# Kernel tuning notes

Measured on AMD Instinct MI355X. Metric: run time of the kernel, lower is better.

The kernel has to match this reference:

```python
import jax, jax.numpy as jnp
import numpy as np

B, S = 128, 512          # batch, sequence length
VOCAB, E, H = 50000, 300, 64  # vocab, embed dim, hidden_size (num conv filters)
KMAX = H // 2 + 2 - 1    # largest kernel height = (H-1)//2 + 2 = 33


def setup_inputs() -> dict:
    key = jax.random.key(0)
    ks = jax.random.split(key, 6)
    x = jax.random.randint(ks[0], (B, 1, S), 0, VOCAB)                  # token ids, [B,1,S]
    emb = jax.random.normal(ks[1], (VOCAB, E), jnp.float32) * 0.1       # frozen embedding table
    Wconv = jax.random.normal(ks[2], (H, KMAX, E), jnp.float32) * 0.05  # padded conv kernels; conv i uses rows [:i//2+2]
    bconv = jax.random.normal(ks[3], (H,), jnp.float32) * 0.05
    Wlin = jax.random.normal(ks[4], (1, H), jnp.float32) * 0.1
    blin = jax.random.normal(ks[5], (1,), jnp.float32) * 0.1
    return {"x": x, "emb": emb, "Wconv": Wconv, "bconv": bconv, "Wlin": Wlin, "blin": blin}


def reference(x, emb, Wconv, bconv, Wlin, blin):
    # Embedding lookup: [B,1,S] -> [B,S,E] (channel dim of 1 is implicit)
    e = emb[x[:, 0]]
    feats = []
    for i in range(H):  # static loop over structurally distinct kernel sizes
        k = i // 2 + 2                      # kernel height for conv i
        w = Wconv[i, :k]                    # [k,E], valid (unpadded) kernel rows
        # Conv2d with kernel (k,E) on [B,1,S,E] == sliding dot product over positions.
        proj = jnp.einsum('bse,ke->bsk', e, w)          # [B,S,k]
        L = S - k + 1                                   # valid output length
        y = sum(proj[:, j:j + L, j] for j in range(k)) + bconv[i]  # [B,L]
        # tanh then topk(k=1, dim=1) == max over positions
        feats.append(jnp.max(jnp.tanh(y), axis=1))      # [B]
    h = jnp.stack(feats, axis=1)                        # [B,H]
    return jax.nn.sigmoid(h @ Wlin.T + blin)            # [B,1]
```

## Files before the change

kernel.cpp:

```cpp
#include <hip/hip_runtime.h>


#define SS     512
#define EE     300
#define HH     64
#define KMAXW  33
#define LP     168
#define HALFSZ 215040

typedef __attribute__((ext_vector_type(8))) short bf16x8;
typedef __attribute__((ext_vector_type(4))) float f32x4;

__device__ __forceinline__ unsigned short f2bf(float f) {
    unsigned u = __float_as_uint(f);
    unsigned r = ((u >> 16) & 1u) + 0x7FFFu;
    return (unsigned short)((u + r) >> 16);
}

__global__ __launch_bounds__(256) void prep_weights(const float* __restrict__ Wconv,
                                                    unsigned short* __restrict__ wsB) {
    int idx = blockIdx.x * 256 + threadIdx.x;
    int r    = idx & 7;
    int lane = (idx >> 3) & 63;
    int gs   = idx >> 9;
    int h    = gs / 420;
    int ww   = gs - h * 420;
    int g, t;
    if      (ww < 45)  { g = 0; t = ww;       }
    else if (ww < 130) { g = 1; t = ww - 45;  }
    else if (ww < 255) { g = 2; t = ww - 130; }
    else               { g = 3; t = ww - 255; }
    int j = t / 5, u = t - j * 5;
    int i  = g * 16 + (lane & 15);
    int ki = i / 2 + 2;
    int kk = (lane >> 4) * 8 + r;
    int e  = h * 160 + u * 32 + kk;
    float v = 0.f;
    if (e < EE && j < ki) v = Wconv[(i * KMAXW + j) * EE + e];
    wsB[idx] = f2bf(v);
}

#define MFMA(A, Bf, C) __builtin_amdgcn_mfma_f32_16x16x32_bf16((A), (Bf), (C), 0, 0, 0)

template<bool SEC>
__device__ __forceinline__ void do5(const unsigned short* lb, int j,
                                    const unsigned short* __restrict__ bp,
                                    int pbase, int sbase, f32x4 acc[3][2]) {
    #pragma unroll
    for (int u = 0; u < 5; ++u) {
        const unsigned short* lr = lb + j * LP + u * 32;
        bf16x8 a0 = *(const bf16x8*)(lr);
        bf16x8 a1 = *(const bf16x8*)(lr + 16 * LP);
        bf16x8 a2 = *(const bf16x8*)(lr + 32 * LP);
        bf16x8 bP = *(const bf16x8*)(bp + (pbase + j * 5 + u) * 512);
        acc[0][0] = MFMA(a0, bP, acc[0][0]);
        acc[1][0] = MFMA(a1, bP, acc[1][0]);
        acc[2][0] = MFMA(a2, bP, acc[2][0]);
        if (SEC) {
            bf16x8 bS = *(const bf16x8*)(bp + (sbase + j * 5 + u) * 512);
            acc[0][1] = MFMA(a0, bS, acc[0][1]);
            acc[1][1] = MFMA(a1, bS, acc[1][1]);
            acc[2][1] = MFMA(a2, bS, acc[2][1]);
        }
    }
}

__global__ __launch_bounds__(256, 3) void conv_fused(const int* __restrict__ x,
                                                     const float* __restrict__ emb,
                                                     const unsigned short* __restrict__ wsB,
                                                     const float* __restrict__ bconv,
                                                     float* __restrict__ wsF) {
    __shared__ __align__(16) unsigned short At[128 * LP];

    int b     = blockIdx.x / 6;
    int slice = blockIdx.x - b * 6;
    int t0    = slice * 96;

    int lane = threadIdx.x & 63;
    int w    = threadIdx.x >> 6;
    int p    = w >> 1;
    int h2   = w & 1;
    int m = lane & 15, q = lane >> 4;

    f32x4 acc[3][2] = {};

    const unsigned short* lb = At + (p * 48 + m) * LP + q * 8;

    for (int eh = 0; eh < 2; ++eh) {
        if (eh) __syncthreads();

        #pragma unroll
        for (int it = 0; it < 10; ++it) {
            int idx = threadIdx.x + it * 256;
            int rr = idx / 20, c = idx - rr * 20;
            int srow = t0 + rr;
            bf16x8 v = {0, 0, 0, 0, 0, 0, 0, 0};
            if (srow < SS) {
                int tok = x[b * SS + srow];
                const float* ep = emb + (long)tok * EE + eh * 160 + c * 8;
                if (eh == 0 || c < 17) {
                    float4 f0 = ((const float4*)ep)[0];
                    float4 f1 = ((const float4*)ep)[1];
                    v[0] = f2bf(f0.x); v[1] = f2bf(f0.y); v[2] = f2bf(f0.z); v[3] = f2bf(f0.w);
                    v[4] = f2bf(f1.x); v[5] = f2bf(f1.y); v[6] = f2bf(f1.z); v[7] = f2bf(f1.w);
                } else if (c == 17) {
                    float4 f0 = ((const float4*)ep)[0];
                    v[0] = f2bf(f0.x); v[1] = f2bf(f0.y); v[2] = f2bf(f0.z); v[3] = f2bf(f0.w);
                }
            }
            *(bf16x8*)&At[rr * LP + c * 8] = v;
        }
        __syncthreads();

        const unsigned short* bp = wsB + eh * HALFSZ + lane * 8;
        if (h2 == 0) {
            #pragma unroll 1
            for (int j = 0; j < 9;  ++j) do5<true >(lb, j, bp, 255, 0, acc);
            #pragma unroll 1
            for (int j = 9; j < 33; ++j) do5<false>(lb, j, bp, 255, 0, acc);
        } else {
            #pragma unroll 1
            for (int j = 0;  j < 17; ++j) do5<true >(lb, j, bp, 130, 45, acc);
            #pragma unroll 1
            for (int j = 17; j < 25; ++j) do5<false>(lb, j, bp, 130, 45, acc);
        }
    }

    int gid[2]; gid[0] = h2 ? 2 : 3; gid[1] = h2 ? 1 : 0;
    #pragma unroll
    for (int t = 0; t < 3; ++t) {
        int tb = t0 + p * 48 + t * 16 + q * 4;
        #pragma unroll
        for (int u2 = 0; u2 < 2; ++u2) {
            int i  = gid[u2] * 16 + m;
            int ki = i / 2 + 2;
            int tmax = SS - ki;
            float bc = bconv[i];
            float mx = -3.0e38f;
            #pragma unroll
            for (int r = 0; r < 4; ++r) {
                float v = tanhf(acc[t][u2][r] + bc);
                if (tb + r <= tmax) mx = fmaxf(mx, v);
            }
            mx = fmaxf(mx, __shfl_xor(mx, 16));
            mx = fmaxf(mx, __shfl_xor(mx, 32));
            if (q == 0) wsF[(b * HH + i) * 36 + slice * 6 + p * 3 + t] = mx;
        }
    }
}

__global__ __launch_bounds__(64) void final_linear(const float* __restrict__ wsF,
                                                   const float* __restrict__ Wlin,
                                                   const float* __restrict__ blin,
                                                   float* __restrict__ out) {
    int b = blockIdx.x;
    int i = threadIdx.x;
    const float* pp = wsF + (b * HH + i) * 36;
    float mx = pp[0];
    #pragma unroll
    for (int j = 1; j < 36; ++j) mx = fmaxf(mx, pp[j]);
    float v = mx * Wlin[i];
    #pragma unroll
    for (int off = 1; off < 64; off <<= 1) v += __shfl_xor(v, off);
    if (i == 0) out[b] = 1.0f / (1.0f + expf(-(v + blin[0])));
}

extern "C" void kernel_launch(void* const* d_in, const int* in_sizes, int n_in,
                              void* d_out, int out_size, void* d_ws, size_t ws_size,
                              hipStream_t stream) {
    const int*   x     = (const int*)d_in[0];
    const float* emb   = (const float*)d_in[1];
    const float* Wconv = (const float*)d_in[2];
    const float* bconv = (const float*)d_in[3];
    const float* Wlin  = (const float*)d_in[4];
    const float* blin  = (const float*)d_in[5];
    float* out = (float*)d_out;

    unsigned short* wsB = (unsigned short*)d_ws;
    float*          wsF = (float*)((char*)d_ws + (1u << 20));

    prep_weights<<<1680, 256, 0, stream>>>(Wconv, wsB);
    conv_fused<<<768, 256, 0, stream>>>(x, emb, wsB, bconv, wsF);
    final_linear<<<128, 64, 0, stream>>>(wsF, Wlin, blin, out);
}
```

Before: 195.2 us.

## Split conv kernel-row loop across wave pairs with LDS reduction of partial sums

Waves in each pair previously split the 64 filters into groups with different kernel lengths, leaving their work uneven. Now each wave takes every other kernel row j for all four filter groups and accumulates into 48 accumulators. The two partial sums are then combined through LDS before tanh and max. This is meant to balance MFMA work between waves and share A-fragment loads across all groups, at the cost of more accumulator registers (which may hurt occupancy), an extra LDS round trip, and a smaller wsF layout.

Measured after the change: 226.2 us. +15.9%, slower.

```diff
diff --git a/kernel.cpp b/kernel.cpp
--- a/kernel.cpp
+++ b/kernel.cpp
@@ -4,7 +4,6 @@
 #define SS     512
 #define EE     300
 #define HH     64
-#define KMAXW  33
 #define LP     168
 #define HALFSZ 215040
 
@@ -36,31 +35,44 @@
     int kk = (lane >> 4) * 8 + r;
     int e  = h * 160 + u * 32 + kk;
     float v = 0.f;
-    if (e < EE && j < ki) v = Wconv[(i * KMAXW + j) * EE + e];
+    if (e < EE && j < ki) v = Wconv[(i * 33 + j) * EE + e];
     wsB[idx] = f2bf(v);
 }
 
 #define MFMA(A, Bf, C) __builtin_amdgcn_mfma_f32_16x16x32_bf16((A), (Bf), (C), 0, 0, 0)
 
-template<bool SEC>
-__device__ __forceinline__ void do5(const unsigned short* lb, int j,
-                                    const unsigned short* __restrict__ bp,
-                                    int pbase, int sbase, f32x4 acc[3][2]) {
+template<int NG>
+__device__ __forceinline__ void stepJ(const unsigned short* lb, int j,
+                                      const unsigned short* __restrict__ bp,
+                                      f32x4 acc[3][4]) {
     #pragma unroll
     for (int u = 0; u < 5; ++u) {
         const unsigned short* lr = lb + j * LP + u * 32;
         bf16x8 a0 = *(const bf16x8*)(lr);
         bf16x8 a1 = *(const bf16x8*)(lr + 16 * LP);
         bf16x8 a2 = *(const bf16x8*)(lr + 32 * LP);
-        bf16x8 bP = *(const bf16x8*)(bp + (pbase + j * 5 + u) * 512);
-        acc[0][0] = MFMA(a0, bP, acc[0][0]);
-        acc[1][0] = MFMA(a1, bP, acc[1][0]);
-        acc[2][0] = MFMA(a2, bP, acc[2][0]);
-        if (SEC) {
-            bf16x8 bS = *(const bf16x8*)(bp + (sbase + j * 5 + u) * 512);
-            acc[0][1] = MFMA(a0, bS, acc[0][1]);
-            acc[1][1] = MFMA(a1, bS, acc[1][1]);
-            acc[2][1] = MFMA(a2, bS, acc[2][1]);
+        int f = j * 5 + u;
+        bf16x8 b3 = *(const bf16x8*)(bp + (255 + f) * 512);
+        acc[0][3] = MFMA(a0, b3, acc[0][3]);
+        acc[1][3] = MFMA(a1, b3, acc[1][3]);
+        acc[2][3] = MFMA(a2, b3, acc[2][3]);
+        if (NG >= 2) {
+            bf16x8 b2 = *(const bf16x8*)(bp + (130 + f) * 512);
+            acc[0][2] = MFMA(a0, b2, acc[0][2]);
+            acc[1][2] = MFMA(a1, b2, acc[1][2]);
+            acc[2][2] = MFMA(a2, b2, acc[2][2]);
+        }
+        if (NG >= 3) {
+            bf16x8 b1 = *(const bf16x8*)(bp + (45 + f) * 512);
+            acc[0][1] = MFMA(a0, b1, acc[0][1]);
+            acc[1][1] = MFMA(a1, b1, acc[1][1]);
+            acc[2][1] = MFMA(a2, b1, acc[2][1]);
+        }
+        if (NG >= 4) {
+            bf16x8 b0 = *(const bf16x8*)(bp + f * 512);
+            acc[0][0] = MFMA(a0, b0, acc[0][0]);
+            acc[1][0] = MFMA(a1, b0, acc[1][0]);
+            acc[2][0] = MFMA(a2, b0, acc[2][0]);
         }
     }
 }
@@ -79,16 +91,14 @@
     int lane = threadIdx.x & 63;
     int w    = threadIdx.x >> 6;
     int p    = w >> 1;
-    int h2   = w & 1;
-    int m = lane & 15, q = lane >> 4;
-
-    f32x4 acc[3][2] = {};
-
-    const unsigned short* lb = At + (p * 48 + m) * LP + q * 8;
+    int q    = w & 1;
+    int m = lane & 15, q16 = lane >> 4;
+
+    f32x4 acc[3][4] = {};
+    const unsigned short* lb = At + (p * 48 + m) * LP + q16 * 8;
 
     for (int eh = 0; eh < 2; ++eh) {
         if (eh) __syncthreads();
-
         #pragma unroll
         for (int it = 0; it < 10; ++it) {
             int idx = threadIdx.x + it * 256;
@@ -113,38 +123,56 @@
         __syncthreads();
 
         const unsigned short* bp = wsB + eh * HALFSZ + lane * 8;
-        if (h2 == 0) {
-            #pragma unroll 1
-            for (int j = 0; j < 9;  ++j) do5<true >(lb, j, bp, 255, 0, acc);
-            #pragma unroll 1
-            for (int j = 9; j < 33; ++j) do5<false>(lb, j, bp, 255, 0, acc);
-        } else {
-            #pragma unroll 1
-            for (int j = 0;  j < 17; ++j) do5<true >(lb, j, bp, 130, 45, acc);
-            #pragma unroll 1
-            for (int j = 17; j < 25; ++j) do5<false>(lb, j, bp, 130, 45, acc);
-        }
-    }
-
-    int gid[2]; gid[0] = h2 ? 2 : 3; gid[1] = h2 ? 1 : 0;
-    #pragma unroll
-    for (int t = 0; t < 3; ++t) {
-        int tb = t0 + p * 48 + t * 16 + q * 4;
-        #pragma unroll
-        for (int u2 = 0; u2 < 2; ++u2) {
-            int i  = gid[u2] * 16 + m;
+        #pragma unroll 1
+        for (int j = q;      j < 9;  j += 2) stepJ<4>(lb, j, bp, acc);
+        #pragma unroll 1
+        for (int j = 10 - q; j < 17; j += 2) stepJ<3>(lb, j, bp, acc);
+        #pragma unroll 1
+        for (int j = 18 - q; j < 25; j += 2) stepJ<2>(lb, j, bp, acc);
+        #pragma unroll 1
+        for (int j = 26 - q; j < 33; j += 2) stepJ<1>(lb, j, bp, acc);
+    }
+
+    __syncthreads();
+    float* red = (float*)At;
+    if (q == 1) {
+        #pragma unroll
+        for (int t = 0; t < 3; ++t)
+            #pragma unroll
+            for (int g = 0; g < 4; ++g)
+                #pragma unroll
+                for (int r = 0; r < 4; ++r)
+                    red[p * 3072 + ((t * 4 + g) * 4 + r) * 64 + lane] = acc[t][g][r];
+    }
+    __syncthreads();
+    if (q == 0) {
+        #pragma unroll
+        for (int t = 0; t < 3; ++t)
+            #pragma unroll
+            for (int g = 0; g < 4; ++g)
+                #pragma unroll
+                for (int r = 0; r < 4; ++r)
+                    acc[t][g][r] += red[p * 3072 + ((t * 4 + g) * 4 + r) * 64 + lane];
+
+        #pragma unroll
+        for (int g = 0; g < 4; ++g) {
+            int i  = g * 16 + m;
             int ki = i / 2 + 2;
             int tmax = SS - ki;
             float bc = bconv[i];
             float mx = -3.0e38f;
             #pragma unroll
-            for (int r = 0; r < 4; ++r) {
-                float v = tanhf(acc[t][u2][r] + bc);
-                if (tb + r <= tmax) mx = fmaxf(mx, v);
+            for (int t = 0; t < 3; ++t) {
+                int tb = t0 + p * 48 + t * 16 + q16 * 4;
+                #pragma unroll
+                for (int r = 0; r < 4; ++r) {
+                    float v = tanhf(acc[t][g][r] + bc);
+                    if (tb + r <= tmax) mx = fmaxf(mx, v);
+                }
             }
             mx = fmaxf(mx, __shfl_xor(mx, 16));
             mx = fmaxf(mx, __shfl_xor(mx, 32));
-            if (q == 0) wsF[(b * HH + i) * 36 + slice * 6 + p * 3 + t] = mx;
+            if (q16 == 0) wsF[(b * HH + i) * 12 + slice * 2 + p] = mx;
         }
     }
 }
@@ -155,10 +183,11 @@
                                                    float* __restrict__ out) {
     int b = blockIdx.x;
     int i = threadIdx.x;
-    const float* pp = wsF + (b * HH + i) * 36;
-    float mx = pp[0];
-    #pragma unroll
-    for (int j = 1; j < 36; ++j) mx = fmaxf(mx, pp[j]);
+    const float4* pp = (const float4*)(wsF + (b * HH + i) * 12);
+    float4 f0 = pp[0], f1 = pp[1], f2 = pp[2];
+    float mx = fmaxf(fmaxf(fmaxf(f0.x, f0.y), fmaxf(f0.z, f0.w)),
+               fmaxf(fmaxf(fmaxf(f1.x, f1.y), fmaxf(f1.z, f1.w)),
+                     fmaxf(fmaxf(f2.x, f2.y), fmaxf(f2.z, f2.w))));
     float v = mx * Wlin[i];
     #pragma unroll
     for (int off = 1; off < 64; off <<= 1) v += __shfl_xor(v, off);
```
